# Performance work log

Hardware: AMD Instinct MI355X
Metric: run time of the kernel (lower is better)

Reference implementation:

```python
import jax, jax.numpy as jnp
import numpy as np

N = 4096      # nodes
E = 65536     # edges (avg degree 16)
NNIN = 64; NEIN = 64; NOPEN = 128; NHID = 128; NCLOSE = 128; NLAYER = 4
H = 0.1; NUM_OUT = 1024; LIN_HID = 256; EPS = 1e-5


def ln_all(x):
    # F.layer_norm(x, x.shape): normalize over ALL elements, no affine
    m = jnp.mean(x)
    v = jnp.mean((x - m) ** 2)
    return (x - m) * jax.lax.rsqrt(v + EPS)


def double_layer(x, K1, K2):
    # edgeConv with 2-D kernel == 1x1 conv == channel mixing
    x = jnp.einsum('oc,bcn->bon', K1, x)
    x = jnp.tanh(ln_all(x))
    return jnp.einsum('oc,bcn->bon', K2, x)


def node_grad(x, I, J, w):      # [1,C,N] -> [1,C,E]
    return w * (x[:, :, I] - x[:, :, J])


def node_ave(x, I, J, w):
    return 0.5 * w * (x[:, :, I] + x[:, :, J])


def edge_div(g, I, J, w, n):    # [1,C,E] -> [1,C,N], signed scatter-add
    wg = w * g
    z = jnp.zeros(g.shape[:2] + (n,), g.dtype)
    return z.at[:, :, I].add(wg).at[:, :, J].add(-wg)


def edge_ave(g, I, J, w, n):    # method='ave'
    wg = w * g
    z = jnp.zeros(g.shape[:2] + (n,), g.dtype)
    return 0.5 * (z.at[:, :, I].add(wg) + z.at[:, :, J].add(wg))


def setup_inputs():
    key = jax.random.key(0)
    ks = jax.random.split(key, 20)
    stdv = 1e-3
    nfeat = 3 * NOPEN  # varlet=False
    return {
        'xn': jax.random.normal(ks[0], (1, NNIN, N), jnp.float32),
        'xe': jax.random.normal(ks[1], (1, NEIN, E), jnp.float32),
        'iInd': jax.random.randint(ks[2], (E,), 0, N),
        'jInd': jax.random.randint(ks[3], (E,), 0, N),
        'K1Nopen': jax.random.normal(ks[4], (NOPEN, NNIN)) * stdv,
        'K2Nopen': jax.random.normal(ks[5], (NOPEN, NOPEN)) * stdv,
        'K1Eopen': jax.random.normal(ks[6], (NOPEN, NEIN)) * stdv,
        'K2Eopen': jax.random.normal(ks[7], (NOPEN, NOPEN)) * stdv,
        'KNclose': jax.random.normal(ks[8], (NCLOSE, NOPEN)) * stdv,
        'KE1': jax.random.uniform(ks[9], (NLAYER, NHID, nfeat)) * stdv,
        'KE2': jax.random.uniform(ks[10], (NLAYER, NOPEN, NHID)) * stdv,
        'KN1': jax.random.uniform(ks[11], (NLAYER, NHID, nfeat)) * stdv,
        'KN2': jax.random.uniform(ks[12], (NLAYER, NOPEN, NHID)) * stdv,
        'W1': jax.random.normal(ks[13], (LIN_HID, NCLOSE)) * 0.02,
        'b1': jnp.zeros((LIN_HID,), jnp.float32),
        'W2': jax.random.normal(ks[14], (NUM_OUT, LIN_HID)) * 0.02,
        'b2': jnp.zeros((NUM_OUT,), jnp.float32),
    }


def reference(xn, xe, iInd, jInd, K1Nopen, K2Nopen, K1Eopen, K2Eopen, KNclose,
              KE1, KE2, KN1, KN2, W1, b1, W2, b2):
    xn = double_layer(xn, K1Nopen, K2Nopen)
    xe = double_layer(xe, K1Eopen, K2Eopen)
    for i in range(NLAYER):
        # periodic pairwise-distance graph reweighting (cdist-style)
        f = xn[0]                                    # [C, N]
        s = jnp.sum(f * f, axis=0)                   # [N]
        D = jax.nn.relu(s[None, :] + s[:, None] - 2.0 * (f.T @ f))  # [N, N]
        D = jnp.exp(-2.0 * D / jnp.std(D, ddof=1))   # torch .std() is unbiased
        w = D[iInd, jInd]                            # [E]
        gradX = node_grad(xn, iInd, jInd, w)
        intX = node_ave(xn, iInd, jInd, w)
        dxe = jnp.concatenate([intX, xe, gradX], axis=1)     # [1, 3*nopen, E]
        dxe = ln_all(double_layer(dxe, KE1[i], KE2[i]))
        xe = xe + H * dxe                                    # wave=True
        divE = edge_div(xe, iInd, jInd, w, N)
        aveE = edge_ave(xe, iInd, jInd, w, N)
        dxn = jnp.concatenate([aveE, divE, xn], axis=1)      # [1, 3*nopen, N]
        dxn = double_layer(dxn, KN1[i], KN2[i])
        xn = xn + H * dxn
    xn = jnp.einsum('oc,bcn->bon', KNclose, xn)  # 1x1 conv close
    x = xn[0].T                                  # [N, nNclose]
    x = jax.nn.elu(x @ W1.T + b1)
    x = x @ W2.T + b2
    return jax.nn.log_softmax(x, axis=1)
```

## Files before the change

### kernel.cpp

```cpp
#include <hip/hip_runtime.h>

#define NNODES 4096
#define NEDGES 65536
#define CH 128

typedef __bf16 bf16x8_t __attribute__((ext_vector_type(8)));
typedef __bf16 bf16x4_t __attribute__((ext_vector_type(4)));
typedef __bf16 bf16x2_t __attribute__((ext_vector_type(2)));
typedef float f32x4_t __attribute__((ext_vector_type(4)));

__device__ __forceinline__ float fast_tanh(float x)
{
  float t = __builtin_amdgcn_exp2f(x * 2.885390081777927f);
  return 1.f - 2.f * __builtin_amdgcn_rcpf(t + 1.f);
}

__device__ __forceinline__ void write_stats(float s, float q, float2* __restrict__ partials,
                                            int pid, int tid, int nwaves)
{
#pragma unroll
  for (int d = 1; d < 64; d <<= 1) { s += __shfl_xor(s, d); q += __shfl_xor(q, d); }
  __shared__ float rs[8][2];
  const int wv = tid >> 6, lane = tid & 63;
  if (lane == 0) { rs[wv][0] = s; rs[wv][1] = q; }
  __syncthreads();
  if (tid == 0) {
    float S = 0.f, Q = 0.f;
    for (int i = 0; i < nwaves; ++i) { S += rs[i][0]; Q += rs[i][1]; }
    partials[pid] = {S, Q};
  }
}

__device__ __forceinline__ float2 params_inline(const float2* __restrict__ pp,
                                                int nblk, double M, int type)
{
  const int tid = threadIdx.x;
  double s = 0.0, q = 0.0;
  for (int i = tid; i < nblk; i += 256) { float2 v = pp[i]; s += (double)v.x; q += (double)v.y; }
#pragma unroll
  for (int d = 1; d < 64; d <<= 1) { s += __shfl_xor(s, d); q += __shfl_xor(q, d); }
  __shared__ double rs4[4], rq4[4];
  __shared__ float pr[2];
  const int wv = tid >> 6, lane = tid & 63;
  if (lane == 0) { rs4[wv] = s; rq4[wv] = q; }
  __syncthreads();
  if (tid == 0) {
    double S = rs4[0] + rs4[1] + rs4[2] + rs4[3];
    double Q = rq4[0] + rq4[1] + rq4[2] + rq4[3];
    if (type == 0) {
      double mean = S / M;
      double var = Q / M - mean * mean;
      if (var < 0.0) var = 0.0;
      pr[0] = (float)mean;
      pr[1] = (float)(1.0 / sqrt(var + 1e-5));
    } else {
      double var = (Q - S * S / M) / (M - 1.0);
      if (var < 1e-30) var = 1e-30;
      pr[0] = (float)(-2.0 / sqrt(var));
      pr[1] = 0.f;
    }
  }
  __syncthreads();
  return {pr[0], pr[1]};
}

template<int EM, int K>
__global__ __launch_bounds__(256) void emfma_k(
    const __bf16* __restrict__ A, const __bf16* __restrict__ X,
    __bf16* __restrict__ Cb,
    float2* __restrict__ partials,
    const __bf16* __restrict__ UVb, const float* __restrict__ wg,
    const int* __restrict__ iIe, const int* __restrict__ jIe,
    const float2* __restrict__ pp, int pnblk, double pM)
{
  float p0 = 0.f, p1 = 0.f;
  if constexpr (EM == 1 || EM == 3) {
    float2 pr = params_inline(pp, pnblk, pM, 0); p0 = pr.x; p1 = pr.y;
  }
  const int tid = threadIdx.x;
  const int wv = tid >> 6, lane = tid & 63;
  const int l15 = lane & 15, ks = lane >> 4;
  const int e = blockIdx.x * 64 + wv * 16 + l15;
  constexpr int KK = K / 32;
  bf16x8_t bq[KK];
  {
    const __bf16* xr = X + (size_t)e * K + ks * 8;
#pragma unroll
    for (int kk = 0; kk < KK; ++kk) {
      bf16x8_t v = *(const bf16x8_t*)(xr + kk * 32);
      if constexpr (EM == 1 || EM == 3) {
#pragma unroll
        for (int j = 0; j < 8; ++j) v[j] = (__bf16)fast_tanh(((float)v[j] - p0) * p1);
      }
      bq[kk] = v;
    }
  }
  float we = 0.f; int ie = 0, je = 0;
  if constexpr (EM == 2) { we = wg[e]; ie = iIe[e]; je = jIe[e]; }
  float dsum = 0.f, dsq = 0.f;
  const int ob0 = blockIdx.y * 4;
#pragma unroll
  for (int obb = 0; obb < 4; ++obb) {
    const int ob = ob0 + obb;
    f32x4_t acc = {0.f, 0.f, 0.f, 0.f};
    const __bf16* ar = A + (size_t)(ob * 16 + l15) * K + ks * 8;
#pragma unroll
    for (int kk = 0; kk < KK; ++kk) {
      bf16x8_t a = *(const bf16x8_t*)(ar + kk * 32);
      acc = __builtin_amdgcn_mfma_f32_16x16x32_bf16(a, bq[kk], acc, 0, 0, 0);
    }
    const int ro = ob * 16 + ks * 4;
    float v0 = acc[0], v1 = acc[1], v2 = acc[2], v3 = acc[3];
    if constexpr (EM == 2) {
      bf16x4_t u4 = *(const bf16x4_t*)&UVb[(size_t)ie * 256 + ro];
      bf16x4_t w4 = *(const bf16x4_t*)&UVb[(size_t)je * 256 + 128 + ro];
      v0 += we * ((float)u4[0] + (float)w4[0]);
      v1 += we * ((float)u4[1] + (float)w4[1]);
      v2 += we * ((float)u4[2] + (float)w4[2]);
      v3 += we * ((float)u4[3] + (float)w4[3]);
    }
    if constexpr (EM != 3) {
      dsum += v0 + v1 + v2 + v3;
      dsq  += v0 * v0 + v1 * v1 + v2 * v2 + v3 * v3;
    }
    bf16x4_t bv;
    bv[0] = (__bf16)v0; bv[1] = (__bf16)v1; bv[2] = (__bf16)v2; bv[3] = (__bf16)v3;
    *(bf16x4_t*)(Cb + (size_t)e * 128 + ro) = bv;
  }
  if constexpr (EM != 3)
    write_stats(dsum, dsq, partials, blockIdx.y * gridDim.x + blockIdx.x, tid, 4);
}

template<int K, bool XSPLIT, bool XT, bool STATS, int OM>
__global__ __launch_bounds__(256) void nmfma_k(
    const __bf16* __restrict__ A, const __bf16* __restrict__ X,
    const __bf16* __restrict__ X2,
    __bf16* __restrict__ Cb, float* __restrict__ Cf, float* __restrict__ resid,
    const float* __restrict__ bias, int nout_stride,
    float2* __restrict__ partials,
    const float2* __restrict__ pp, int pnblk, double pM)
{
  float p0 = 0.f, p1 = 0.f;
  if constexpr (XT) { float2 pr = params_inline(pp, pnblk, pM, 0); p0 = pr.x; p1 = pr.y; }
  const int tid = threadIdx.x;
  const int wv = tid >> 6, lane = tid & 63;
  const int l15 = lane & 15, ks = lane >> 4;
  const int n = blockIdx.x * 64 + wv * 16 + l15;
  constexpr int KK = K / 32;
  bf16x8_t bq[KK];
  if constexpr (XSPLIT) {
    const __bf16* xr  = X  + (size_t)n * 256 + ks * 8;
    const __bf16* xr2 = X2 + (size_t)n * 128 + ks * 8;
#pragma unroll
    for (int kk = 0; kk < 8; ++kk) bq[kk] = *(const bf16x8_t*)(xr + kk * 32);
#pragma unroll
    for (int kk = 8; kk < KK; ++kk) bq[kk] = *(const bf16x8_t*)(xr2 + (kk - 8) * 32);
  } else {
    const __bf16* xr = X + (size_t)n * K + ks * 8;
#pragma unroll
    for (int kk = 0; kk < KK; ++kk) {
      bf16x8_t v = *(const bf16x8_t*)(xr + kk * 32);
      if constexpr (XT) {
#pragma unroll
        for (int j = 0; j < 8; ++j) v[j] = (__bf16)fast_tanh(((float)v[j] - p0) * p1);
      }
      bq[kk] = v;
    }
  }
  float dsum = 0.f, dsq = 0.f;
  const int ob0 = blockIdx.y * 4;
#pragma unroll
  for (int obb = 0; obb < 4; ++obb) {
    const int ob = ob0 + obb;
    f32x4_t acc = {0.f, 0.f, 0.f, 0.f};
    const __bf16* ar = A + (size_t)(ob * 16 + l15) * K + ks * 8;
#pragma unroll
    for (int kk = 0; kk < KK; ++kk) {
      bf16x8_t a = *(const bf16x8_t*)(ar + kk * 32);
      acc = __builtin_amdgcn_mfma_f32_16x16x32_bf16(a, bq[kk], acc, 0, 0, 0);
    }
    const int ro = ob * 16 + ks * 4;
    float v[4] = {acc[0], acc[1], acc[2], acc[3]};
    if constexpr (OM == 1 || OM == 2) {
#pragma unroll
      for (int r = 0; r < 4; ++r) v[r] += bias[ro + r];
    }
    if constexpr (OM == 1) {
#pragma unroll
      for (int r = 0; r < 4; ++r) v[r] = v[r] > 0.f ? v[r] : expm1f(v[r]);
    }
    if constexpr (STATS) {
#pragma unroll
      for (int r = 0; r < 4; ++r) { dsum += v[r]; dsq += v[r] * v[r]; }
    }
    if constexpr (OM == 4) {
      float4* rp = (float4*)&resid[(size_t)n * 128 + ro];
      float4 rr = *rp;
      rr.x += 0.1f * v[0]; rr.y += 0.1f * v[1]; rr.z += 0.1f * v[2]; rr.w += 0.1f * v[3];
      *rp = rr;
    } else if constexpr (OM == 2 || OM == 3) {
      float4 fv = {v[0], v[1], v[2], v[3]};
      *(float4*)(Cf + (size_t)n * nout_stride + ro) = fv;
    } else {
      bf16x4_t bv;
      bv[0] = (__bf16)v[0]; bv[1] = (__bf16)v[1]; bv[2] = (__bf16)v[2]; bv[3] = (__bf16)v[3];
      *(bf16x4_t*)(Cb + (size_t)n * nout_stride + ro) = bv;
    }
  }
  if constexpr (STATS)
    write_stats(dsum, dsq, partials, blockIdx.y * gridDim.x + blockIdx.x, tid, 4);
}

__global__ __launch_bounds__(256) void dstat_k(
    const __bf16* __restrict__ fT, const float* __restrict__ s,
    float2* __restrict__ partials)
{
  int rem = blockIdx.x, i0t = 0;
  while (rem >= 64 - i0t) { rem -= 64 - i0t; ++i0t; }
  const int i0 = i0t * 64, j0 = (i0t + rem) * 64;
  const float wgt = (j0 > i0) ? 2.f : 1.f;
  const int tid = threadIdx.x;
  const int wv = tid >> 6, lane = tid & 63, l15 = lane & 15, ks = lane >> 4;
  const int irow = i0 + wv * 16 + l15;
  bf16x8_t aq[4];
  const __bf16* ar = fT + (size_t)irow * 128 + ks * 8;
#pragma unroll
  for (int kk = 0; kk < 4; ++kk) aq[kk] = *(const bf16x8_t*)(ar + kk * 32);
  float si[4];
#pragma unroll
  for (int r = 0; r < 4; ++r) si[r] = s[i0 + wv * 16 + ks * 4 + r];
  float dsum = 0.f, dsq = 0.f;
#pragma unroll
  for (int jb = 0; jb < 4; ++jb) {
    const int jcol = j0 + jb * 16 + l15;
    const __bf16* br = fT + (size_t)jcol * 128 + ks * 8;
    f32x4_t acc = {0.f, 0.f, 0.f, 0.f};
#pragma unroll
    for (int kk = 0; kk < 4; ++kk) {
      bf16x8_t b = *(const bf16x8_t*)(br + kk * 32);
      acc = __builtin_amdgcn_mfma_f32_16x16x32_bf16(aq[kk], b, acc, 0, 0, 0);
    }
    const float sj = s[jcol];
#pragma unroll
    for (int r = 0; r < 4; ++r) {
      float d = si[r] + sj - 2.f * acc[r];
      d = d > 0.f ? d : 0.f;
      dsum += d; dsq += d * d;
    }
  }
  write_stats(dsum * wgt, dsq * wgt, partials, blockIdx.x, tid, 4);
}

__global__ __launch_bounds__(256) void bcvt_k(const float* __restrict__ xnN,
                                              __bf16* __restrict__ xnNb,
                                              float* __restrict__ sbuf)
{
  const int n = blockIdx.x * 64 + (threadIdx.x >> 2);
  const int q = (threadIdx.x & 3) * 32;
  const float* src = xnN + (size_t)n * 128 + q;
  __bf16* dst = xnNb + (size_t)n * 128 + q;
  float ss = 0.f;
#pragma unroll
  for (int j = 0; j < 8; ++j) {
    float4 v = *(const float4*)(src + 4 * j);
    bf16x4_t b;
    b[0] = (__bf16)v.x; b[1] = (__bf16)v.y; b[2] = (__bf16)v.z; b[3] = (__bf16)v.w;
    float f0 = (float)b[0], f1 = (float)b[1], f2 = (float)b[2], f3 = (float)b[3];
    ss += f0 * f0 + f1 * f1 + f2 * f2 + f3 * f3;
    *(bf16x4_t*)(dst + 4 * j) = b;
  }
  ss += __shfl_xor(ss, 1);
  ss += __shfl_xor(ss, 2);
  if ((threadIdx.x & 3) == 0) sbuf[n] = ss;
}

__global__ __launch_bounds__(256) void etrans_k(const float* __restrict__ src,
                                                __bf16* __restrict__ dst, int ncols)
{
  __shared__ float t[64][65];
  const int e0 = blockIdx.x * 64;
  const int tx = threadIdx.x & 63, tw = threadIdx.x >> 6;
  for (int c = tw; c < 64; c += 4)
    t[tx][c] = src[(size_t)c * ncols + e0 + tx];
  __syncthreads();
  const int el = threadIdx.x >> 2, c0 = (threadIdx.x & 3) * 16;
  for (int q = 0; q < 4; ++q) {
    int c = c0 + q * 4;
    bf16x4_t b;
    b[0] = (__bf16)t[el][c];     b[1] = (__bf16)t[el][c + 1];
    b[2] = (__bf16)t[el][c + 2]; b[3] = (__bf16)t[el][c + 3];
    *(bf16x4_t*)&dst[(size_t)(e0 + el) * 64 + c] = b;
  }
}

__global__ __launch_bounds__(256) void edge_w_k(
    const __bf16* __restrict__ xnNb, const float* __restrict__ s,
    const int* __restrict__ iI, const int* __restrict__ jJ,
    const float2* __restrict__ pp, float* __restrict__ w)
{
  float2 pr = params_inline(pp, 2080, (double)NNODES * (double)NNODES, 1);
  const float factor = pr.x;
  int e = blockIdx.x * 256 + threadIdx.x;
  int a = iI[e], b = jJ[e];
  const bf16x8_t* pa = (const bf16x8_t*)(xnNb + (size_t)a * CH);
  const bf16x8_t* pb = (const bf16x8_t*)(xnNb + (size_t)b * CH);
  float g = 0.f;
#pragma unroll
  for (int q = 0; q < CH / 8; ++q) {
    bf16x8_t u = pa[q], v = pb[q];
#pragma unroll
    for (int j = 0; j < 8; ++j) g = fmaf((float)u[j], (float)v[j], g);
  }
  float d = s[a] + s[b] - 2.f * g;
  d = d > 0.f ? d : 0.f;
  w[e] = __builtin_amdgcn_exp2f(factor * d * 1.4426950408889634f);
}

__global__ void wcvt_k(const float* __restrict__ K1E, const float* __restrict__ K2E,
                       const float* __restrict__ KE1, const float* __restrict__ KE2,
                       const float* __restrict__ KNc, const float* __restrict__ W1,
                       const float* __restrict__ W2, const float* __restrict__ KN1,
                       const float* __restrict__ KN2, const float* __restrict__ K1N,
                       const float* __restrict__ K2N,
                       __bf16* __restrict__ K1Eb, __bf16* __restrict__ K2Eb,
                       __bf16* __restrict__ KE1b, __bf16* __restrict__ KE2b,
                       __bf16* __restrict__ KNcb, __bf16* __restrict__ W1b,
                       __bf16* __restrict__ W2b, __bf16* __restrict__ KN1b,
                       __bf16* __restrict__ KN2b, __bf16* __restrict__ a1a2b,
                       __bf16* __restrict__ K1Nb, __bf16* __restrict__ K2Nb)
{
  int id = blockIdx.x * 256 + threadIdx.x;
  if (id < 8192) { K1Eb[id] = (__bf16)K1E[id]; return; }
  id -= 8192;
  if (id < 16384) { K2Eb[id] = (__bf16)K2E[id]; return; }
  id -= 16384;
  if (id < 65536) {
    int l = id >> 14, rem = id & 16383, r = rem >> 7, c = rem & 127;
    KE1b[id] = (__bf16)KE1[(size_t)l * 49152 + r * 384 + 128 + c];
    return;
  }
  id -= 65536;
  if (id < 65536) { KE2b[id] = (__bf16)KE2[id]; return; }
  id -= 65536;
  if (id < 16384) { KNcb[id] = (__bf16)KNc[id]; return; }
  id -= 16384;
  if (id < 32768) { W1b[id] = (__bf16)W1[id]; return; }
  id -= 32768;
  if (id < 262144) { W2b[id] = (__bf16)W2[id]; return; }
  id -= 262144;
  if (id < 196608) { KN1b[id] = (__bf16)KN1[id]; return; }
  id -= 196608;
  if (id < 65536) { KN2b[id] = (__bf16)KN2[id]; return; }
  id -= 65536;
  if (id < 131072) {
    int l = id >> 15, rem = id & 32767, r = rem >> 7, c = rem & 127;
    int o = r & 127;
    float k1 = KE1[(size_t)l * 49152 + o * 384 + c];
    float k3 = KE1[(size_t)l * 49152 + o * 384 + 256 + c];
    a1a2b[id] = (__bf16)((r < 128) ? (0.5f * k1 + k3) : (0.5f * k1 - k3));
    return;
  }
  id -= 131072;
  if (id < 8192) { K1Nb[id] = (__bf16)K1N[id]; return; }
  id -= 8192;
  if (id < 16384) { K2Nb[id] = (__bf16)K2N[id]; return; }
}

__global__ __launch_bounds__(256) void lnres_k(
    const __bf16* __restrict__ eBT, __bf16* __restrict__ xeT,
    const float2* __restrict__ pp)
{
  float2 pr = params_inline(pp, 2048, (double)CH * NEDGES, 0);
  const float m = pr.x, r = pr.y;
  const size_t base = (size_t)blockIdx.x * (256 * 16);
  for (int it = 0; it < 2; ++it) {
    size_t i = base + (size_t)it * 2048 + (size_t)threadIdx.x * 8;
    bf16x8_t b = *(const bf16x8_t*)(eBT + i);
    bf16x8_t x = *(const bf16x8_t*)(xeT + i);
    bf16x8_t ob;
#pragma unroll
    for (int j = 0; j < 8; ++j)
      ob[j] = (__bf16)((float)x[j] + 0.1f * (((float)b[j] - m) * r));
    *(bf16x8_t*)(xeT + i) = ob;
  }
}

__global__ void hist_k(const int* __restrict__ iI, const int* __restrict__ jJ,
                       int* __restrict__ cnt)
{
  int e = blockIdx.x * 256 + threadIdx.x;
  atomicAdd(&cnt[iI[e]], 1);
  atomicAdd(&cnt[jJ[e]], 1);
}

__global__ __launch_bounds__(1024) void scan_k(const int* __restrict__ cnt,
                                               int* __restrict__ offs,
                                               int* __restrict__ cursor)
{
  __shared__ int tmp[1024];
  const int tid = threadIdx.x;
  int4 v = *(const int4*)&cnt[tid * 4];
  int s = v.x + v.y + v.z + v.w;
  tmp[tid] = s; __syncthreads();
  for (int d = 1; d < 1024; d <<= 1) {
    int t = (tid >= d) ? tmp[tid - d] : 0;
    __syncthreads();
    tmp[tid] += t;
    __syncthreads();
  }
  int base = tmp[tid] - s;
  int4 o = {base, base + v.x, base + v.x + v.y, base + v.x + v.y + v.z};
  *(int4*)&offs[tid * 4] = o;
  *(int4*)&cursor[tid * 4] = o;
  if (tid == 1023) offs[4096] = tmp[1023];
}

__global__ void fill_k(const int* __restrict__ iI, const int* __restrict__ jJ,
                       int* __restrict__ cursor, int* __restrict__ list)
{
  int e = blockIdx.x * 256 + threadIdx.x;
  int p1 = atomicAdd(&cursor[iI[e]], 1);
  list[p1] = e;
  int p2 = atomicAdd(&cursor[jJ[e]], 1);
  list[p2] = e | 0x80000000;
}

__global__ __launch_bounds__(512) void gather_k(
    const __bf16* __restrict__ xeT, const float* __restrict__ w,
    const int* __restrict__ offs, const int* __restrict__ list,
    __bf16* __restrict__ catb)
{
  __shared__ float comb[4][4][64];
  const int wv = threadIdx.x >> 6, lane = threadIdx.x & 63;
  const int nn = wv >> 1, half = wv & 1;
  const int n = blockIdx.x * 4 + nn;
  const int k0 = offs[n], k1 = offs[n + 1];
  float s1a = 0.f, s1b = 0.f, s2a = 0.f, s2b = 0.f;
#pragma unroll 2
  for (int k = k0 + half; k < k1; k += 2) {
    int enc = list[k];
    int e = enc & 0x7fffffff;
    float we = w[e];
    bf16x2_t xv = *(const bf16x2_t*)&xeT[(size_t)e * 128 + lane * 2];
    float va = (float)xv[0] * we;
    float vb = (float)xv[1] * we;
    if (enc >= 0) { s1a += va; s1b += vb; }
    else          { s2a += va; s2b += vb; }
  }
  if (half == 1) {
    comb[nn][0][lane] = s1a; comb[nn][1][lane] = s1b;
    comb[nn][2][lane] = s2a; comb[nn][3][lane] = s2b;
  }
  __syncthreads();
  if (half == 0) {
    s1a += comb[nn][0][lane]; s1b += comb[nn][1][lane];
    s2a += comb[nn][2][lane]; s2b += comb[nn][3][lane];
    __bf16* row = catb + (size_t)n * 256;
    bf16x2_t av, dv;
    av[0] = (__bf16)(0.5f * (s1a + s2a)); av[1] = (__bf16)(0.5f * (s1b + s2b));
    dv[0] = (__bf16)(s1a - s2a);          dv[1] = (__bf16)(s1b - s2b);
    *(bf16x2_t*)&row[lane * 2] = av;
    *(bf16x2_t*)&row[128 + lane * 2] = dv;
  }
}

__global__ __launch_bounds__(256) void logsoftmax_k(float* __restrict__ out)
{
  __shared__ float red[256];
  const int n = blockIdx.x, tid = threadIdx.x;
  float* row = out + (size_t)n * 1024;
  float v[4];
  float mx = -1e30f;
#pragma unroll
  for (int l = 0; l < 4; ++l) { v[l] = row[tid + 256 * l]; mx = fmaxf(mx, v[l]); }
  red[tid] = mx; __syncthreads();
  for (int s = 128; s > 0; s >>= 1) { if (tid < s) red[tid] = fmaxf(red[tid], red[tid + s]); __syncthreads(); }
  float m = red[0]; __syncthreads();
  float se = 0.f;
#pragma unroll
  for (int l = 0; l < 4; ++l) se += expf(v[l] - m);
  red[tid] = se; __syncthreads();
  for (int s = 128; s > 0; s >>= 1) { if (tid < s) red[tid] += red[tid + s]; __syncthreads(); }
  float L = m + logf(red[0]);
#pragma unroll
  for (int l = 0; l < 4; ++l) row[tid + 256 * l] = v[l] - L;
}

extern "C" void kernel_launch(void* const* d_in, const int* in_sizes, int n_in,
                              void* d_out, int out_size, void* d_ws, size_t ws_size,
                              hipStream_t stream)
{
  (void)in_sizes; (void)n_in; (void)out_size; (void)ws_size;
  const float* xn_in = (const float*)d_in[0];
  const float* xe_in = (const float*)d_in[1];
  const int*   iI    = (const int*)d_in[2];
  const int*   jJ    = (const int*)d_in[3];
  const float* K1N   = (const float*)d_in[4];
  const float* K2N   = (const float*)d_in[5];
  const float* K1E   = (const float*)d_in[6];
  const float* K2E   = (const float*)d_in[7];
  const float* KNc   = (const float*)d_in[8];
  const float* KE1   = (const float*)d_in[9];
  const float* KE2   = (const float*)d_in[10];
  const float* KN1   = (const float*)d_in[11];
  const float* KN2   = (const float*)d_in[12];
  const float* W1    = (const float*)d_in[13];
  const float* b1    = (const float*)d_in[14];
  const float* W2    = (const float*)d_in[15];
  const float* b2    = (const float*)d_in[16];
  float* out = (float*)d_out;

  float* ws = (float*)d_ws;
  size_t off = 0;
  auto alloc = [&](size_t n) { size_t o = off; off += (n + 63) & ~(size_t)63; return o; };
  float* xnN   = ws + alloc((size_t)NNODES * CH);
  __bf16* xeT  = (__bf16*)(ws + alloc((size_t)NEDGES * CH / 2));
  __bf16* eAT  = (__bf16*)(ws + alloc((size_t)NEDGES * CH / 2));
  __bf16* eBT  = (__bf16*)(ws + alloc((size_t)NEDGES * CH / 2));
  float* sbuf  = ws + alloc(NNODES);
  float* wbuf  = ws + alloc(NEDGES);
  __bf16* UVb  = (__bf16*)(ws + alloc((size_t)NNODES * 256 / 2));
  __bf16* xnNb = (__bf16*)(ws + alloc((size_t)NNODES * CH / 2));
  __bf16* catb = (__bf16*)(ws + alloc((size_t)NNODES * 256 / 2));
  __bf16* nAb  = (__bf16*)(ws + alloc((size_t)NNODES * CH / 2));
  __bf16* zb   = (__bf16*)(ws + alloc((size_t)NNODES * CH / 2));
  __bf16* l1bb = (__bf16*)(ws + alloc((size_t)NNODES * 256 / 2));
  __bf16* K1Eb = (__bf16*)(ws + alloc(8192 / 2));
  __bf16* K2Eb = (__bf16*)(ws + alloc(16384 / 2));
  __bf16* KE1b = (__bf16*)(ws + alloc(65536 / 2));
  __bf16* KE2b = (__bf16*)(ws + alloc(65536 / 2));
  __bf16* KNcb = (__bf16*)(ws + alloc(16384 / 2));
  __bf16* W1b  = (__bf16*)(ws + alloc(32768 / 2));
  __bf16* W2b  = (__bf16*)(ws + alloc(262144 / 2));
  __bf16* KN1b = (__bf16*)(ws + alloc(196608 / 2));
  __bf16* KN2b = (__bf16*)(ws + alloc(65536 / 2));
  __bf16* a1a2b= (__bf16*)(ws + alloc(131072 / 2));
  __bf16* K1Nb = (__bf16*)(ws + alloc(8192 / 2));
  __bf16* K2Nb = (__bf16*)(ws + alloc(16384 / 2));
  int* csr_cnt    = (int*)(ws + alloc(4096));
  int* csr_offs   = (int*)(ws + alloc(4160));
  int* csr_cursor = (int*)(ws + alloc(4096));
  int* csr_list   = (int*)(ws + alloc(2 * NEDGES));
  float2* pA = (float2*)(ws + alloc((size_t)4096 * 2));
  float2* pB = (float2*)(ws + alloc((size_t)4096 * 2));
  __bf16* xeT64  = eBT;
  __bf16* xnT64b = UVb;

  const __bf16* BNUL = nullptr;
  const float* NUL = nullptr;
  const int* NULI = nullptr;
  const float2* PNUL = nullptr;

  wcvt_k<<<3456, 256, 0, stream>>>(K1E, K2E, KE1, KE2, KNc, W1, W2, KN1, KN2, K1N, K2N,
                                   K1Eb, K2Eb, KE1b, KE2b, KNcb, W1b, W2b, KN1b, KN2b,
                                   a1a2b, K1Nb, K2Nb);
  hipMemsetAsync(csr_cnt, 0, 4096 * sizeof(int), stream);
  hist_k<<<NEDGES / 256, 256, 0, stream>>>(iI, jJ, csr_cnt);
  scan_k<<<1, 1024, 0, stream>>>(csr_cnt, csr_offs, csr_cursor);
  fill_k<<<NEDGES / 256, 256, 0, stream>>>(iI, jJ, csr_cursor, csr_list);

  etrans_k<<<NNODES / 64, 256, 0, stream>>>(xn_in, xnT64b, NNODES);
  nmfma_k<64, false, false, true, 0><<<dim3(64, 2), 256, 0, stream>>>(
      K1Nb, xnT64b, BNUL, nAb, nullptr, nullptr, NUL, 128, pA, PNUL, 0, 0.0);
  nmfma_k<128, false, true, false, 3><<<dim3(64, 2), 256, 0, stream>>>(
      K2Nb, nAb, BNUL, nullptr, xnN, nullptr, NUL, 128, nullptr,
      pA, 128, (double)CH * NNODES);

  etrans_k<<<NEDGES / 64, 256, 0, stream>>>(xe_in, xeT64, NEDGES);
  emfma_k<0, 64><<<dim3(NEDGES / 64, 2), 256, 0, stream>>>(K1Eb, xeT64, eAT,
      pA, BNUL, NUL, NULI, NULI, PNUL, 0, 0.0);
  emfma_k<3, 128><<<dim3(NEDGES / 64, 2), 256, 0, stream>>>(K2Eb, eAT, xeT,
      nullptr, BNUL, NUL, NULI, NULI, pA, 2048, (double)CH * NEDGES);

  for (int i = 0; i < 4; ++i) {
    const __bf16* KE1bi = KE1b + (size_t)i * 128 * 128;
    const __bf16* KE2bi = KE2b + (size_t)i * 128 * 128;
    const __bf16* KN1bi = KN1b + (size_t)i * 128 * 384;
    const __bf16* KN2bi = KN2b + (size_t)i * 128 * 128;
    const __bf16* a1a2i = a1a2b + (size_t)i * 256 * 128;

    bcvt_k<<<NNODES / 64, 256, 0, stream>>>(xnN, xnNb, sbuf);
    dstat_k<<<2080, 256, 0, stream>>>(xnNb, sbuf, pA);
    edge_w_k<<<NEDGES / 256, 256, 0, stream>>>(xnNb, sbuf, iI, jJ, pA, wbuf);

    nmfma_k<128, false, false, false, 0><<<dim3(64, 4), 256, 0, stream>>>(
        a1a2i, xnNb, BNUL, UVb, nullptr, nullptr, NUL, 256, nullptr, PNUL, 0, 0.0);
    emfma_k<2, 128><<<dim3(NEDGES / 64, 2), 256, 0, stream>>>(KE1bi, xeT, eAT,
        pB, UVb, wbuf, iI, jJ, PNUL, 0, 0.0);
    emfma_k<1, 128><<<dim3(NEDGES / 64, 2), 256, 0, stream>>>(KE2bi, eAT, eBT,
        pA, BNUL, NUL, NULI, NULI, pB, 2048, (double)CH * NEDGES);
    lnres_k<<<2048, 256, 0, stream>>>(eBT, xeT, pA);

    gather_k<<<NNODES / 4, 512, 0, stream>>>(xeT, wbuf, csr_offs, csr_list, catb);
    nmfma_k<384, true, false, true, 0><<<dim3(64, 2), 256, 0, stream>>>(
        KN1bi, catb, xnNb, nAb, nullptr, nullptr, NUL, 128, pB, PNUL, 0, 0.0);
    nmfma_k<128, false, true, false, 4><<<dim3(64, 2), 256, 0, stream>>>(
        KN2bi, nAb, BNUL, nullptr, nullptr, xnN, NUL, 128, nullptr,
        pB, 128, (double)CH * NNODES);
  }

  bcvt_k<<<NNODES / 64, 256, 0, stream>>>(xnN, xnNb, sbuf);
  nmfma_k<128, false, false, false, 0><<<dim3(64, 2), 256, 0, stream>>>(
      KNcb, xnNb, BNUL, zb, nullptr, nullptr, NUL, 128, nullptr, PNUL, 0, 0.0);
  nmfma_k<128, false, false, false, 1><<<dim3(64, 4), 256, 0, stream>>>(
      W1b, zb, BNUL, l1bb, nullptr, nullptr, b1, 256, nullptr, PNUL, 0, 0.0);
  nmfma_k<256, false, false, false, 2><<<dim3(64, 16), 256, 0, stream>>>(
      W2b, l1bb, BNUL, nullptr, out, nullptr, b2, 1024, nullptr, PNUL, 0, 0.0);
  logsoftmax_k<<<NNODES, 256, 0, stream>>>(out);
}
```

Measured before the change: 698.2 us.

## Fuse edge MLP stages into cooperative grid-synced kernels and drop bf16 convert pass

Replaces the separate edge-weight, two edge MFMA, and layer-norm residual kernels with one cooperative kernel per layer. It keeps intermediate edge activations in shared memory and uses grid.sync to finalize the global layer-norm statistics between stages. It also computes the edge weights inside that kernel, and has the node residual kernel emit the bf16 copy and per-node squared norms directly, removing the separate bcvt pass. This cuts launches and round trips of 65536x128 intermediates through HBM. The cost is grid-wide barriers and a 1024-block cooperative launch that must be fully co-resident, which limits occupancy and can fail if residency is not met.

```diff
diff --git a/kernel.cpp b/kernel.cpp
--- a/kernel.cpp
+++ b/kernel.cpp
@@ -1,8 +1,11 @@
 #include <hip/hip_runtime.h>
+#include <hip/hip_cooperative_groups.h>
 
 #define NNODES 4096
 #define NEDGES 65536
 #define CH 128
+
+namespace cg = cooperative_groups;
 
 typedef __bf16 bf16x8_t __attribute__((ext_vector_type(8)));
 typedef __bf16 bf16x4_t __attribute__((ext_vector_type(4)));
@@ -64,81 +67,193 @@
   return {pr[0], pr[1]};
 }
 
-template<int EM, int K>
-__global__ __launch_bounds__(256) void emfma_k(
-    const __bf16* __restrict__ A, const __bf16* __restrict__ X,
-    __bf16* __restrict__ Cb,
-    float2* __restrict__ partials,
-    const __bf16* __restrict__ UVb, const float* __restrict__ wg,
-    const int* __restrict__ iIe, const int* __restrict__ jIe,
-    const float2* __restrict__ pp, int pnblk, double pM)
-{
-  float p0 = 0.f, p1 = 0.f;
-  if constexpr (EM == 1 || EM == 3) {
-    float2 pr = params_inline(pp, pnblk, pM, 0); p0 = pr.x; p1 = pr.y;
-  }
+__global__ __launch_bounds__(256, 4) void oedge_k(
+    const __bf16* __restrict__ K1Eb, const __bf16* __restrict__ K2Eb,
+    const __bf16* __restrict__ xeT64, __bf16* __restrict__ xeT,
+    float2* __restrict__ pS)
+{
+  __shared__ __bf16 eAl[64 * 132];
+  cg::grid_group grid = cg::this_grid();
   const int tid = threadIdx.x;
   const int wv = tid >> 6, lane = tid & 63;
   const int l15 = lane & 15, ks = lane >> 4;
-  const int e = blockIdx.x * 64 + wv * 16 + l15;
-  constexpr int KK = K / 32;
-  bf16x8_t bq[KK];
+  const int row = wv * 16 + l15;
+  const int e = blockIdx.x * 64 + row;
+
+  bf16x8_t bq[2];
   {
-    const __bf16* xr = X + (size_t)e * K + ks * 8;
-#pragma unroll
-    for (int kk = 0; kk < KK; ++kk) {
-      bf16x8_t v = *(const bf16x8_t*)(xr + kk * 32);
-      if constexpr (EM == 1 || EM == 3) {
-#pragma unroll
-        for (int j = 0; j < 8; ++j) v[j] = (__bf16)fast_tanh(((float)v[j] - p0) * p1);
-      }
-      bq[kk] = v;
-    }
-  }
-  float we = 0.f; int ie = 0, je = 0;
-  if constexpr (EM == 2) { we = wg[e]; ie = iIe[e]; je = jIe[e]; }
+    const __bf16* xr = xeT64 + (size_t)e * 64 + ks * 8;
+    bq[0] = *(const bf16x8_t*)(xr);
+    bq[1] = *(const bf16x8_t*)(xr + 32);
+  }
   float dsum = 0.f, dsq = 0.f;
-  const int ob0 = blockIdx.y * 4;
-#pragma unroll
-  for (int obb = 0; obb < 4; ++obb) {
-    const int ob = ob0 + obb;
+#pragma unroll
+  for (int ob = 0; ob < 8; ++ob) {
     f32x4_t acc = {0.f, 0.f, 0.f, 0.f};
-    const __bf16* ar = A + (size_t)(ob * 16 + l15) * K + ks * 8;
-#pragma unroll
-    for (int kk = 0; kk < KK; ++kk) {
-      bf16x8_t a = *(const bf16x8_t*)(ar + kk * 32);
-      acc = __builtin_amdgcn_mfma_f32_16x16x32_bf16(a, bq[kk], acc, 0, 0, 0);
-    }
+    const __bf16* ar = K1Eb + (size_t)(ob * 16 + l15) * 64 + ks * 8;
+    acc = __builtin_amdgcn_mfma_f32_16x16x32_bf16(*(const bf16x8_t*)(ar), bq[0], acc, 0, 0, 0);
+    acc = __builtin_amdgcn_mfma_f32_16x16x32_bf16(*(const bf16x8_t*)(ar + 32), bq[1], acc, 0, 0, 0);
     const int ro = ob * 16 + ks * 4;
     float v0 = acc[0], v1 = acc[1], v2 = acc[2], v3 = acc[3];
-    if constexpr (EM == 2) {
-      bf16x4_t u4 = *(const bf16x4_t*)&UVb[(size_t)ie * 256 + ro];
-      bf16x4_t w4 = *(const bf16x4_t*)&UVb[(size_t)je * 256 + 128 + ro];
-      v0 += we * ((float)u4[0] + (float)w4[0]);
-      v1 += we * ((float)u4[1] + (float)w4[1]);
-      v2 += we * ((float)u4[2] + (float)w4[2]);
-      v3 += we * ((float)u4[3] + (float)w4[3]);
-    }
-    if constexpr (EM != 3) {
-      dsum += v0 + v1 + v2 + v3;
-      dsq  += v0 * v0 + v1 * v1 + v2 * v2 + v3 * v3;
-    }
+    dsum += v0 + v1 + v2 + v3;
+    dsq  += v0 * v0 + v1 * v1 + v2 * v2 + v3 * v3;
     bf16x4_t bv;
     bv[0] = (__bf16)v0; bv[1] = (__bf16)v1; bv[2] = (__bf16)v2; bv[3] = (__bf16)v3;
-    *(bf16x4_t*)(Cb + (size_t)e * 128 + ro) = bv;
-  }
-  if constexpr (EM != 3)
-    write_stats(dsum, dsq, partials, blockIdx.y * gridDim.x + blockIdx.x, tid, 4);
-}
-
-template<int K, bool XSPLIT, bool XT, bool STATS, int OM>
+    *(bf16x4_t*)(eAl + row * 132 + ro) = bv;
+  }
+  write_stats(dsum, dsq, pS, blockIdx.x, tid, 4);
+  grid.sync();
+
+  float2 p1 = params_inline(pS, 1024, (double)CH * NEDGES, 0);
+  bf16x8_t bq2[4];
+#pragma unroll
+  for (int kk = 0; kk < 4; ++kk) {
+    bf16x8_t v = *(const bf16x8_t*)(eAl + row * 132 + ks * 8 + kk * 32);
+#pragma unroll
+    for (int j = 0; j < 8; ++j) v[j] = (__bf16)fast_tanh(((float)v[j] - p1.x) * p1.y);
+    bq2[kk] = v;
+  }
+#pragma unroll
+  for (int ob = 0; ob < 8; ++ob) {
+    f32x4_t acc = {0.f, 0.f, 0.f, 0.f};
+    const __bf16* ar = K2Eb + (size_t)(ob * 16 + l15) * CH + ks * 8;
+#pragma unroll
+    for (int kk = 0; kk < 4; ++kk)
+      acc = __builtin_amdgcn_mfma_f32_16x16x32_bf16(*(const bf16x8_t*)(ar + kk * 32), bq2[kk], acc, 0, 0, 0);
+    const int ro = ob * 16 + ks * 4;
+    bf16x4_t bv;
+    bv[0] = (__bf16)acc[0]; bv[1] = (__bf16)acc[1];
+    bv[2] = (__bf16)acc[2]; bv[3] = (__bf16)acc[3];
+    *(bf16x4_t*)(xeT + (size_t)e * CH + ro) = bv;
+  }
+}
+
+__global__ __launch_bounds__(256, 4) void fedge_k(
+    const __bf16* __restrict__ KE1bi, const __bf16* __restrict__ KE2bi,
+    __bf16* __restrict__ xeT, const __bf16* __restrict__ UVb,
+    const __bf16* __restrict__ xnNb, const float* __restrict__ sbufh,
+    const int* __restrict__ iI, const int* __restrict__ jJ,
+    float* __restrict__ wbuf,
+    const float2* __restrict__ pD, float2* __restrict__ pSA, float2* __restrict__ pSB)
+{
+  __shared__ __bf16 eAl[64 * 132];
+  __shared__ __bf16 xel[64 * 132];
+  __shared__ float wl[64];
+  cg::grid_group grid = cg::this_grid();
+  const int tid = threadIdx.x;
+  const int wv = tid >> 6, lane = tid & 63;
+  const int l15 = lane & 15, ks = lane >> 4;
+  const int row = wv * 16 + l15;
+  const int e = blockIdx.x * 64 + row;
+
+  float2 fp = params_inline(pD, 2080, (double)NNODES * (double)NNODES, 1);
+  {
+    const int eg = blockIdx.x * 64 + (tid >> 2);
+    const int a = iI[eg], b = jJ[eg];
+    const bf16x8_t* pa = (const bf16x8_t*)(xnNb + (size_t)a * CH + (tid & 3) * 32);
+    const bf16x8_t* pb = (const bf16x8_t*)(xnNb + (size_t)b * CH + (tid & 3) * 32);
+    float g = 0.f;
+#pragma unroll
+    for (int q = 0; q < 4; ++q) {
+      bf16x8_t u = pa[q], v = pb[q];
+#pragma unroll
+      for (int j = 0; j < 8; ++j) g = fmaf((float)u[j], (float)v[j], g);
+    }
+    g += __shfl_xor(g, 1); g += __shfl_xor(g, 2);
+    float d = sbufh[a] + sbufh[NNODES + a] + sbufh[b] + sbufh[NNODES + b] - 2.f * g;
+    d = d > 0.f ? d : 0.f;
+    float wgt = __builtin_amdgcn_exp2f(fp.x * d * 1.4426950408889634f);
+    if ((tid & 3) == 0) { wl[tid >> 2] = wgt; wbuf[eg] = wgt; }
+  }
+  __syncthreads();
+
+  const int ie = iI[e], je = jJ[e];
+  const float we = wl[row];
+  bf16x8_t bq[4];
+  {
+    const __bf16* xr = xeT + (size_t)e * CH + ks * 8;
+#pragma unroll
+    for (int kk = 0; kk < 4; ++kk) {
+      bf16x8_t v = *(const bf16x8_t*)(xr + kk * 32);
+      bq[kk] = v;
+      *(bf16x8_t*)(xel + row * 132 + ks * 8 + kk * 32) = v;
+    }
+  }
+  float dsum = 0.f, dsq = 0.f;
+#pragma unroll
+  for (int ob = 0; ob < 8; ++ob) {
+    f32x4_t acc = {0.f, 0.f, 0.f, 0.f};
+    const __bf16* ar = KE1bi + (size_t)(ob * 16 + l15) * CH + ks * 8;
+#pragma unroll
+    for (int kk = 0; kk < 4; ++kk)
+      acc = __builtin_amdgcn_mfma_f32_16x16x32_bf16(*(const bf16x8_t*)(ar + kk * 32), bq[kk], acc, 0, 0, 0);
+    const int ro = ob * 16 + ks * 4;
+    bf16x4_t u4 = *(const bf16x4_t*)&UVb[(size_t)ie * 256 + ro];
+    bf16x4_t w4 = *(const bf16x4_t*)&UVb[(size_t)je * 256 + 128 + ro];
+    float v0 = acc[0] + we * ((float)u4[0] + (float)w4[0]);
+    float v1 = acc[1] + we * ((float)u4[1] + (float)w4[1]);
+    float v2 = acc[2] + we * ((float)u4[2] + (float)w4[2]);
+    float v3 = acc[3] + we * ((float)u4[3] + (float)w4[3]);
+    dsum += v0 + v1 + v2 + v3;
+    dsq  += v0 * v0 + v1 * v1 + v2 * v2 + v3 * v3;
+    bf16x4_t bv;
+    bv[0] = (__bf16)v0; bv[1] = (__bf16)v1; bv[2] = (__bf16)v2; bv[3] = (__bf16)v3;
+    *(bf16x4_t*)(eAl + row * 132 + ro) = bv;
+  }
+  write_stats(dsum, dsq, pSA, blockIdx.x, tid, 4);
+  grid.sync();
+
+  float2 p1 = params_inline(pSA, 1024, (double)CH * NEDGES, 0);
+  bf16x8_t bq2[4];
+#pragma unroll
+  for (int kk = 0; kk < 4; ++kk) {
+    bf16x8_t v = *(const bf16x8_t*)(eAl + row * 132 + ks * 8 + kk * 32);
+#pragma unroll
+    for (int j = 0; j < 8; ++j) v[j] = (__bf16)fast_tanh(((float)v[j] - p1.x) * p1.y);
+    bq2[kk] = v;
+  }
+  __syncthreads();
+  dsum = 0.f; dsq = 0.f;
+#pragma unroll
+  for (int ob = 0; ob < 8; ++ob) {
+    f32x4_t acc = {0.f, 0.f, 0.f, 0.f};
+    const __bf16* ar = KE2bi + (size_t)(ob * 16 + l15) * CH + ks * 8;
+#pragma unroll
+    for (int kk = 0; kk < 4; ++kk)
+      acc = __builtin_amdgcn_mfma_f32_16x16x32_bf16(*(const bf16x8_t*)(ar + kk * 32), bq2[kk], acc, 0, 0, 0);
+    const int ro = ob * 16 + ks * 4;
+    float v0 = acc[0], v1 = acc[1], v2 = acc[2], v3 = acc[3];
+    dsum += v0 + v1 + v2 + v3;
+    dsq  += v0 * v0 + v1 * v1 + v2 * v2 + v3 * v3;
+    bf16x4_t bv;
+    bv[0] = (__bf16)v0; bv[1] = (__bf16)v1; bv[2] = (__bf16)v2; bv[3] = (__bf16)v3;
+    *(bf16x4_t*)(eAl + row * 132 + ro) = bv;
+  }
+  write_stats(dsum, dsq, pSB, blockIdx.x, tid, 4);
+  grid.sync();
+
+  float2 p2 = params_inline(pSB, 1024, (double)CH * NEDGES, 0);
+#pragma unroll
+  for (int kk = 0; kk < 4; ++kk) {
+    bf16x8_t b8 = *(const bf16x8_t*)(eAl + row * 132 + ks * 8 + kk * 32);
+    bf16x8_t x8 = *(const bf16x8_t*)(xel + row * 132 + ks * 8 + kk * 32);
+    bf16x8_t o8;
+#pragma unroll
+    for (int j = 0; j < 8; ++j)
+      o8[j] = (__bf16)((float)x8[j] + 0.1f * (((float)b8[j] - p2.x) * p2.y));
+    *(bf16x8_t*)(xeT + (size_t)e * CH + ks * 8 + kk * 32) = o8;
+  }
+}
+
+template<int K, bool XSPLIT, bool XT, bool STATS, int OM, bool EMITB>
 __global__ __launch_bounds__(256) void nmfma_k(
     const __bf16* __restrict__ A, const __bf16* __restrict__ X,
     const __bf16* __restrict__ X2,
     __bf16* __restrict__ Cb, float* __restrict__ Cf, float* __restrict__ resid,
     const float* __restrict__ bias, int nout_stride,
     float2* __restrict__ partials,
-    const float2* __restrict__ pp, int pnblk, double pM)
+    const float2* __restrict__ pp, int pnblk, double pM,
+    __bf16* __restrict__ xbout, float* __restrict__ shout)
 {
   float p0 = 0.f, p1 = 0.f;
   if constexpr (XT) { float2 pr = params_inline(pp, pnblk, pM, 0); p0 = pr.x; p1 = pr.y; }
@@ -167,7 +282,7 @@
       bq[kk] = v;
     }
   }
-  float dsum = 0.f, dsq = 0.f;
+  float dsum = 0.f, dsq = 0.f, ss = 0.f;
   const int ob0 = blockIdx.y * 4;
 #pragma unroll
   for (int obb = 0; obb < 4; ++obb) {
@@ -198,21 +313,40 @@
       float4 rr = *rp;
       rr.x += 0.1f * v[0]; rr.y += 0.1f * v[1]; rr.z += 0.1f * v[2]; rr.w += 0.1f * v[3];
       *rp = rr;
+      if constexpr (EMITB) {
+        bf16x4_t eb;
+        eb[0] = (__bf16)rr.x; eb[1] = (__bf16)rr.y; eb[2] = (__bf16)rr.z; eb[3] = (__bf16)rr.w;
+        *(bf16x4_t*)(xbout + (size_t)n * 128 + ro) = eb;
+#pragma unroll
+        for (int r = 0; r < 4; ++r) { float f = (float)eb[r]; ss += f * f; }
+      }
     } else if constexpr (OM == 2 || OM == 3) {
       float4 fv = {v[0], v[1], v[2], v[3]};
       *(float4*)(Cf + (size_t)n * nout_stride + ro) = fv;
+      if constexpr (EMITB) {
+        bf16x4_t eb;
+        eb[0] = (__bf16)v[0]; eb[1] = (__bf16)v[1]; eb[2] = (__bf16)v[2]; eb[3] = (__bf16)v[3];
+        *(bf16x4_t*)(xbout + (size_t)n * 128 + ro) = eb;
+#pragma unroll
+        for (int r = 0; r < 4; ++r) { float f = (float)eb[r]; ss += f * f; }
+      }
     } else {
       bf16x4_t bv;
       bv[0] = (__bf16)v[0]; bv[1] = (__bf16)v[1]; bv[2] = (__bf16)v[2]; bv[3] = (__bf16)v[3];
       *(bf16x4_t*)(Cb + (size_t)n * nout_stride + ro) = bv;
     }
   }
+  if constexpr (EMITB) {
+    ss += __shfl_xor(ss, 16);
+    ss += __shfl_xor(ss, 32);
+    if (lane < 16) shout[blockIdx.y * NNODES + n] = ss;
+  }
   if constexpr (STATS)
     write_stats(dsum, dsq, partials, blockIdx.y * gridDim.x + blockIdx.x, tid, 4);
 }
 
 __global__ __launch_bounds__(256) void dstat_k(
-    const __bf16* __restrict__ fT, const float* __restrict__ s,
+    const __bf16* __restrict__ fT, const float* __restrict__ sh,
     float2* __restrict__ partials)
 {
   int rem = blockIdx.x, i0t = 0;
@@ -228,7 +362,10 @@
   for (int kk = 0; kk < 4; ++kk) aq[kk] = *(const bf16x8_t*)(ar + kk * 32);
   float si[4];
 #pragma unroll
-  for (int r = 0; r < 4; ++r) si[r] = s[i0 + wv * 16 + ks * 4 + r];
+  for (int r = 0; r < 4; ++r) {
+    int ii = i0 + wv * 16 + ks * 4 + r;
+    si[r] = sh[ii] + sh[NNODES + ii];
+  }
   float dsum = 0.f, dsq = 0.f;
 #pragma unroll
   for (int jb = 0; jb < 4; ++jb) {
@@ -240,7 +377,7 @@
       bf16x8_t b = *(const bf16x8_t*)(br + kk * 32);
       acc = __builtin_amdgcn_mfma_f32_16x16x32_bf16(aq[kk], b, acc, 0, 0, 0);
     }
-    const float sj = s[jcol];
+    const float sj = sh[jcol] + sh[NNODES + jcol];
 #pragma unroll
     for (int r = 0; r < 4; ++r) {
       float d = si[r] + sj - 2.f * acc[r];
@@ -249,29 +386,6 @@
     }
   }
   write_stats(dsum * wgt, dsq * wgt, partials, blockIdx.x, tid, 4);
-}
-
-__global__ __launch_bounds__(256) void bcvt_k(const float* __restrict__ xnN,
-                                              __bf16* __restrict__ xnNb,
-                                              float* __restrict__ sbuf)
-{
-  const int n = blockIdx.x * 64 + (threadIdx.x >> 2);
-  const int q = (threadIdx.x & 3) * 32;
-  const float* src = xnN + (size_t)n * 128 + q;
-  __bf16* dst = xnNb + (size_t)n * 128 + q;
-  float ss = 0.f;
-#pragma unroll
-  for (int j = 0; j < 8; ++j) {
-    float4 v = *(const float4*)(src + 4 * j);
-    bf16x4_t b;
-    b[0] = (__bf16)v.x; b[1] = (__bf16)v.y; b[2] = (__bf16)v.z; b[3] = (__bf16)v.w;
-    float f0 = (float)b[0], f1 = (float)b[1], f2 = (float)b[2], f3 = (float)b[3];
-    ss += f0 * f0 + f1 * f1 + f2 * f2 + f3 * f3;
-    *(bf16x4_t*)(dst + 4 * j) = b;
-  }
-  ss += __shfl_xor(ss, 1);
-  ss += __shfl_xor(ss, 2);
-  if ((threadIdx.x & 3) == 0) sbuf[n] = ss;
 }
 
 __global__ __launch_bounds__(256) void etrans_k(const float* __restrict__ src,
@@ -291,29 +405,6 @@
     b[2] = (__bf16)t[el][c + 2]; b[3] = (__bf16)t[el][c + 3];
     *(bf16x4_t*)&dst[(size_t)(e0 + el) * 64 + c] = b;
   }
-}
-
-__global__ __launch_bounds__(256) void edge_w_k(
-    const __bf16* __restrict__ xnNb, const float* __restrict__ s,
-    const int* __restrict__ iI, const int* __restrict__ jJ,
-    const float2* __restrict__ pp, float* __restrict__ w)
-{
-  float2 pr = params_inline(pp, 2080, (double)NNODES * (double)NNODES, 1);
-  const float factor = pr.x;
-  int e = blockIdx.x * 256 + threadIdx.x;
-  int a = iI[e], b = jJ[e];
-  const bf16x8_t* pa = (const bf16x8_t*)(xnNb + (size_t)a * CH);
-  const bf16x8_t* pb = (const bf16x8_t*)(xnNb + (size_t)b * CH);
-  float g = 0.f;
-#pragma unroll
-  for (int q = 0; q < CH / 8; ++q) {
-    bf16x8_t u = pa[q], v = pb[q];
-#pragma unroll
-    for (int j = 0; j < 8; ++j) g = fmaf((float)u[j], (float)v[j], g);
-  }
-  float d = s[a] + s[b] - 2.f * g;
-  d = d > 0.f ? d : 0.f;
-  w[e] = __builtin_amdgcn_exp2f(factor * d * 1.4426950408889634f);
 }
 
 __global__ void wcvt_k(const float* __restrict__ K1E, const float* __restrict__ K2E,
@@ -366,25 +457,6 @@
   if (id < 16384) { K2Nb[id] = (__bf16)K2N[id]; return; }
 }
 
-__global__ __launch_bounds__(256) void lnres_k(
-    const __bf16* __restrict__ eBT, __bf16* __restrict__ xeT,
-    const float2* __restrict__ pp)
-{
-  float2 pr = params_inline(pp, 2048, (double)CH * NEDGES, 0);
-  const float m = pr.x, r = pr.y;
-  const size_t base = (size_t)blockIdx.x * (256 * 16);
-  for (int it = 0; it < 2; ++it) {
-    size_t i = base + (size_t)it * 2048 + (size_t)threadIdx.x * 8;
-    bf16x8_t b = *(const bf16x8_t*)(eBT + i);
-    bf16x8_t x = *(const bf16x8_t*)(xeT + i);
-    bf16x8_t ob;
-#pragma unroll
-    for (int j = 0; j < 8; ++j)
-      ob[j] = (__bf16)((float)x[j] + 0.1f * (((float)b[j] - m) * r));
-    *(bf16x8_t*)(xeT + i) = ob;
-  }
-}
-
 __global__ void hist_k(const int* __restrict__ iI, const int* __restrict__ jJ,
                        int* __restrict__ cnt)
 {
@@ -515,9 +587,8 @@
   auto alloc = [&](size_t n) { size_t o = off; off += (n + 63) & ~(size_t)63; return o; };
   float* xnN   = ws + alloc((size_t)NNODES * CH);
   __bf16* xeT  = (__bf16*)(ws + alloc((size_t)NEDGES * CH / 2));
-  __bf16* eAT  = (__bf16*)(ws + alloc((size_t)NEDGES * CH / 2));
-  __bf16* eBT  = (__bf16*)(ws + alloc((size_t)NEDGES * CH / 2));
-  float* sbuf  = ws + alloc(NNODES);
+  __bf16* xeT64= (__bf16*)(ws + alloc((size_t)NEDGES * 64 / 2));
+  float* sbufh = ws + alloc(2 * NNODES);
   float* wbuf  = ws + alloc(NEDGES);
   __bf16* UVb  = (__bf16*)(ws + alloc((size_t)NNODES * 256 / 2));
   __bf16* xnNb = (__bf16*)(ws + alloc((size_t)NNODES * CH / 2));
@@ -543,13 +614,14 @@
   int* csr_list   = (int*)(ws + alloc(2 * NEDGES));
   float2* pA = (float2*)(ws + alloc((size_t)4096 * 2));
   float2* pB = (float2*)(ws + alloc((size_t)4096 * 2));
-  __bf16* xeT64  = eBT;
+  float2* pC = (float2*)(ws + alloc((size_t)4096 * 2));
   __bf16* xnT64b = UVb;
 
   const __bf16* BNUL = nullptr;
   const float* NUL = nullptr;
-  const int* NULI = nullptr;
   const float2* PNUL = nullptr;
+  __bf16* BNULm = nullptr;
+  float* NULm = nullptr;
 
   wcvt_k<<<3456, 256, 0, stream>>>(K1E, K2E, KE1, KE2, KNc, W1, W2, KN1, KN2, K1N, K2N,
                                    K1Eb, K2Eb, KE1b, KE2b, KNcb, W1b, W2b, KN1b, KN2b,
@@ -560,17 +632,20 @@
   fill_k<<<NEDGES / 256, 256, 0, stream>>>(iI, jJ, csr_cursor, csr_list);
 
   etrans_k<<<NNODES / 64, 256, 0, stream>>>(xn_in, xnT64b, NNODES);
-  nmfma_k<64, false, false, true, 0><<<dim3(64, 2), 256, 0, stream>>>(
-      K1Nb, xnT64b, BNUL, nAb, nullptr, nullptr, NUL, 128, pA, PNUL, 0, 0.0);
-  nmfma_k<128, false, true, false, 3><<<dim3(64, 2), 256, 0, stream>>>(
+  nmfma_k<64, false, false, true, 0, false><<<dim3(64, 2), 256, 0, stream>>>(
+      K1Nb, xnT64b, BNUL, nAb, nullptr, nullptr, NUL, 128, pA, PNUL, 0, 0.0, BNULm, NULm);
+  nmfma_k<128, false, true, false, 3, true><<<dim3(64, 2), 256, 0, stream>>>(
       K2Nb, nAb, BNUL, nullptr, xnN, nullptr, NUL, 128, nullptr,
-      pA, 128, (double)CH * NNODES);
+      pA, 128, (double)CH * NNODES, xnNb, sbufh);
 
   etrans_k<<<NEDGES / 64, 256, 0, stream>>>(xe_in, xeT64, NEDGES);
-  emfma_k<0, 64><<<dim3(NEDGES / 64, 2), 256, 0, stream>>>(K1Eb, xeT64, eAT,
-      pA, BNUL, NUL, NULI, NULI, PNUL, 0, 0.0);
-  emfma_k<3, 128><<<dim3(NEDGES / 64, 2), 256, 0, stream>>>(K2Eb, eAT, xeT,
-      nullptr, BNUL, NUL, NULI, NULI, pA, 2048, (double)CH * NEDGES);
+  {
+    const __bf16* a0 = K1Eb; const __bf16* a1 = K2Eb;
+    const __bf16* a2 = xeT64; __bf16* a3 = xeT; float2* a4 = pB;
+    void* args[] = {&a0, &a1, &a2, &a3, &a4};
+    hipLaunchCooperativeKernel((const void*)oedge_k, dim3(NEDGES / 64), dim3(256),
+                               args, 0, stream);
+  }
 
   for (int i = 0; i < 4; ++i) {
     const __bf16* KE1bi = KE1b + (size_t)i * 128 * 128;
@@ -579,32 +654,34 @@
     const __bf16* KN2bi = KN2b + (size_t)i * 128 * 128;
     const __bf16* a1a2i = a1a2b + (size_t)i * 256 * 128;
 
-    bcvt_k<<<NNODES / 64, 256, 0, stream>>>(xnN, xnNb, sbuf);
-    dstat_k<<<2080, 256, 0, stream>>>(xnNb, sbuf, pA);
-    edge_w_k<<<NEDGES / 256, 256, 0, stream>>>(xnNb, sbuf, iI, jJ, pA, wbuf);
-
-    nmfma_k<128, false, false, false, 0><<<dim3(64, 4), 256, 0, stream>>>(
-        a1a2i, xnNb, BNUL, UVb, nullptr, nullptr, NUL, 256, nullptr, PNUL, 0, 0.0);
-    emfma_k<2, 128><<<dim3(NEDGES / 64, 2), 256, 0, stream>>>(KE1bi, xeT, eAT,
-        pB, UVb, wbuf, iI, jJ, PNUL, 0, 0.0);
-    emfma_k<1, 128><<<dim3(NEDGES / 64, 2), 256, 0, stream>>>(KE2bi, eAT, eBT,
-        pA, BNUL, NUL, NULI, NULI, pB, 2048, (double)CH * NEDGES);
-    lnres_k<<<2048, 256, 0, stream>>>(eBT, xeT, pA);
+    dstat_k<<<2080, 256, 0, stream>>>(xnNb, sbufh, pA);
+
+    nmfma_k<128, false, false, false, 0, false><<<dim3(64, 4), 256, 0, stream>>>(
+        a1a2i, xnNb, BNUL, UVb, nullptr, nullptr, NUL, 256, nullptr, PNUL, 0, 0.0, BNULm, NULm);
+
+    {
+      const __bf16* f0 = KE1bi; const __bf16* f1 = KE2bi;
+      __bf16* f2 = xeT; const __bf16* f3 = UVb; const __bf16* f4 = xnNb;
+      const float* f5 = sbufh; const int* f6 = iI; const int* f7 = jJ;
+      float* f8 = wbuf; const float2* f9 = pA; float2* f10 = pB; float2* f11 = pC;
+      void* args[] = {&f0, &f1, &f2, &f3, &f4, &f5, &f6, &f7, &f8, &f9, &f10, &f11};
+      hipLaunchCooperativeKernel((const void*)fedge_k, dim3(NEDGES / 64), dim3(256),
+                                 args, 0, stream);
+    }
 
     gather_k<<<NNODES / 4, 512, 0, stream>>>(xeT, wbuf, csr_offs, csr_list, catb);
-    nmfma_k<384, true, false, true, 0><<<dim3(64, 2), 256, 0, stream>>>(
-        KN1bi, catb, xnNb, nAb, nullptr, nullptr, NUL, 128, pB, PNUL, 0, 0.0);
-    nmfma_k<128, false, true, false, 4><<<dim3(64, 2), 256, 0, stream>>>(
+    nmfma_k<384, true, false, true, 0, false><<<dim3(64, 2), 256, 0, stream>>>(
+        KN1bi, catb, xnNb, nAb, nullptr, nullptr, NUL, 128, pB, PNUL, 0, 0.0, BNULm, NULm);
+    nmfma_k<128, false, true, false, 4, true><<<dim3(64, 2), 256, 0, stream>>>(
         KN2bi, nAb, BNUL, nullptr, nullptr, xnN, NUL, 128, nullptr,
-        pB, 128, (double)CH * NNODES);
-  }
-
-  bcvt_k<<<NNODES / 64, 256, 0, stream>>>(xnN, xnNb, sbuf);
-  nmfma_k<128, false, false, false, 0><<<dim3(64, 2), 256, 0, stream>>>(
-      KNcb, xnNb, BNUL, zb, nullptr, nullptr, NUL, 128, nullptr, PNUL, 0, 0.0);
-  nmfma_k<128, false, false, false, 1><<<dim3(64, 4), 256, 0, stream>>>(
-      W1b, zb, BNUL, l1bb, nullptr, nullptr, b1, 256, nullptr, PNUL, 0, 0.0);
-  nmfma_k<256, false, false, false, 2><<<dim3(64, 16), 256, 0, stream>>>(
-      W2b, l1bb, BNUL, nullptr, out, nullptr, b2, 1024, nullptr, PNUL, 0, 0.0);
+        pB, 128, (double)CH * NNODES, xnNb, sbufh);
+  }
+
+  nmfma_k<128, false, false, false, 0, false><<<dim3(64, 2), 256, 0, stream>>>(
+      KNcb, xnNb, BNUL, zb, nullptr, nullptr, NUL, 128, nullptr, PNUL, 0, 0.0, BNULm, NULm);
+  nmfma_k<128, false, false, false, 1, false><<<dim3(64, 4), 256, 0, stream>>>(
+      W1b, zb, BNUL, l1bb, nullptr, nullptr, b1, 256, nullptr, PNUL, 0, 0.0, BNULm, NULm);
+  nmfma_k<256, false, false, false, 2, false><<<dim3(64, 16), 256, 0, stream>>>(
+      W2b, l1bb, BNUL, nullptr, out, nullptr, b2, 1024, nullptr, PNUL, 0, 0.0, BNULm, NULm);
   logsoftmax_k<<<NNODES, 256, 0, stream>>>(out);
 }
```

Result: slower. 1.535 ms (+119.8%).
